# Performance work log

Measured on AMD Instinct MI355X. Metric: run time of the kernel, lower is better.

Reference implementation:

```python
import jax, jax.numpy as jnp
import numpy as np

NB, DIN, DOUT = 4, 1024, 256
B, S = 8, 2048

def setup_inputs() -> dict:
    key = jax.random.key(0)
    ks = jax.random.split(key, 9)
    sd_in = 1.0 / np.sqrt(DIN)
    sd_cat = 1.0 / np.sqrt(DOUT * NB)
    return {
        'x':  jax.random.normal(ks[0], (B, S, DIN), jnp.float32),
        'Wq': jax.random.normal(ks[1], (NB, DIN, DOUT), jnp.float32) * sd_in,
        'bq': jax.random.normal(ks[2], (NB, DOUT), jnp.float32) * 0.01,
        'Wk': jax.random.normal(ks[3], (NB, DIN, DOUT), jnp.float32) * sd_in,
        'bk': jax.random.normal(ks[4], (NB, DOUT), jnp.float32) * 0.01,
        'Wv': jax.random.normal(ks[5], (NB, DIN, DOUT), jnp.float32) * sd_in,
        'bv': jax.random.normal(ks[6], (NB, DOUT), jnp.float32) * 0.01,
        'Wo': jax.random.normal(ks[7], (NB * DOUT, DOUT), jnp.float32) * sd_cat,
        'bo': jnp.zeros((DOUT,), jnp.float32),
    }

def reference(x, Wq, bq, Wk, bk, Wv, bv, Wo, bo):
    # Per-block linear projections, all blocks vectorized: [nb, b, s, d]
    Q = jnp.einsum('bsi,nio->nbso', x, Wq) + bq[:, None, None, :]
    K = jnp.einsum('bsi,nio->nbso', x, Wk) + bk[:, None, None, :]
    V = jnp.einsum('bsi,nio->nbso', x, Wv) + bv[:, None, None, :]
    scale = 1.0 / np.sqrt(DOUT)
    scores = jnp.einsum('nbso,nbto->nbst', Q, K) * scale  # [nb,b,s,s]
    weights = jax.nn.softmax(scores, axis=-1)
    attn = jnp.einsum('nbst,nbto->nbso', weights, V)       # [nb,b,s,d]
    # concat blocks along last dim: [b,s,nb*d]
    combined = jnp.transpose(attn, (1, 2, 0, 3)).reshape(attn.shape[1], attn.shape[2], -1)
    return combined @ Wo + bo
```

## Files before the change

### kernel.cpp

```cpp
#include <hip/hip_runtime.h>
#include <hip/hip_bf16.h>

typedef __attribute__((ext_vector_type(8))) short bf16x8;
typedef __attribute__((ext_vector_type(4))) float f32x4;
typedef __attribute__((ext_vector_type(16))) float f32x16;

#define DEVI __device__ __forceinline__

DEVI unsigned short f2bf(float f) {
  union { float f; unsigned u; } v; v.f = f;
  unsigned r = v.u + 0x7FFFu + ((v.u >> 16) & 1u);
  return (unsigned short)(r >> 16);
}

DEVI unsigned cvtpk(float lo, float hi) {
  unsigned r;
  asm("v_cvt_pk_bf16_f32 %0, %1, %2" : "=v"(r) : "v"(lo), "v"(hi));
  return r;
}

DEVI void gload16(const void* g, void* l) {
  __builtin_amdgcn_global_load_lds(
      (const __attribute__((address_space(1))) unsigned int*)g,
      (__attribute__((address_space(3))) unsigned int*)l, 16, 0, 0);
}

__global__ void k_prep(const float* __restrict__ x, unsigned short* __restrict__ xb,
                       const float* __restrict__ Wq, const float* __restrict__ Wk,
                       const float* __restrict__ Wv, const float* __restrict__ Wo,
                       unsigned short* __restrict__ Wt, unsigned short* __restrict__ Wot) {
  __shared__ float t[32][33];
  int bid = blockIdx.x;
  if (bid < 2048) {
    int i = bid * 256 + threadIdx.x;
    const int stride = 2048 * 256;
#pragma unroll
    for (int it = 0; it < 8; ++it, i += stride) {
      float4 v = ((const float4*)x)[i];
      ushort4 o;
      o.x = f2bf(v.x); o.y = f2bf(v.y); o.z = f2bf(v.z); o.w = f2bf(v.w);
      ((ushort4*)xb)[i] = o;
    }
  } else {
    int b2 = bid - 2048;
    int z = b2 >> 8, rem = b2 & 255;
    int r0 = (rem >> 3) * 32, c0 = (rem & 7) * 32;
    const float* in = z < 4 ? Wq : (z < 8 ? Wk : (z < 12 ? Wv : Wo));
    size_t ibase = (size_t)(z < 12 ? (z & 3) : 0) * 262144;
    unsigned short* out = z < 12 ? (Wt + (size_t)z * 262144) : Wot;
    int tx = threadIdx.x & 31, ty = threadIdx.x >> 5;
    for (int i = 0; i < 32; i += 8)
      t[ty + i][tx] = in[ibase + (size_t)(r0 + ty + i) * 256 + (c0 + tx)];
    __syncthreads();
    for (int i = 0; i < 32; i += 8)
      out[(size_t)(c0 + ty + i) * 1024 + (r0 + tx)] = f2bf(t[tx][ty + i]);
  }
}

__global__ __launch_bounds__(256, 3) void k_gemmqkv(
    const unsigned short* __restrict__ A,
    const unsigned short* __restrict__ B,
    const float* __restrict__ bq, const float* __restrict__ bk,
    const float* __restrict__ bv,
    unsigned short* __restrict__ Qb, unsigned short* __restrict__ Kg,
    unsigned short* __restrict__ Vt, float qscale)
{
  __shared__ unsigned short As[128 * 64];
  __shared__ unsigned short Bs[128 * 64];
  int tid = threadIdx.x;
  int w = tid >> 6, l = tid & 63;
  int lg = l >> 4, lm = l & 15;
  int wr = w >> 1, wc = w & 1;
  int bid = blockIdx.x;
  int wg = (bid & 7) * 384 + (bid >> 3);
  int rowblk = wg / 24, colblk = wg % 24;
  int row0 = rowblk * 128, col0 = colblk * 128;

  const f32x4 fz = {0.f, 0.f, 0.f, 0.f};
  f32x4 acc[4][4];
  for (int i = 0; i < 4; i++) for (int j = 0; j < 4; j++) acc[i][j] = fz;

  for (int t = 0; t < 16; ++t) {
    int k0 = t << 6;
    __syncthreads();
#pragma unroll
    for (int j = 0; j < 4; ++j) {
      int ch = j * 256 + tid;
      int row = ch >> 3, cirp = (ch & 7) ^ (row & 7);
      gload16(A + (size_t)(row0 + row) * 1024 + k0 + cirp * 8,
              As + (size_t)(j * 256 + w * 64) * 8);
      gload16(B + (size_t)(col0 + row) * 1024 + k0 + cirp * 8,
              Bs + (size_t)(j * 256 + w * 64) * 8);
    }
    __syncthreads();
#pragma unroll
    for (int kt = 0; kt < 2; ++kt) {
      bf16x8 bfr[4];
#pragma unroll
      for (int ni = 0; ni < 4; ++ni) {
        int r = wc * 64 + ni * 16 + lm;
        bfr[ni] = *(const bf16x8*)((const char*)Bs + r * 128 + ((kt * 64 + lg * 16) ^ ((r & 7) << 4)));
      }
#pragma unroll
      for (int mi = 0; mi < 4; ++mi) {
        int r = wr * 64 + mi * 16 + lm;
        bf16x8 afr = *(const bf16x8*)((const char*)As + r * 128 + ((kt * 64 + lg * 16) ^ ((r & 7) << 4)));
#pragma unroll
        for (int ni = 0; ni < 4; ++ni)
          acc[mi][ni] = __builtin_amdgcn_mfma_f32_16x16x32_bf16(afr, bfr[ni], acc[mi][ni], 0, 0, 0);
      }
    }
  }

  int sel = col0 >> 10;
  const float* bb = sel == 0 ? bq : (sel == 1 ? bk : bv);
#pragma unroll
  for (int mi = 0; mi < 4; ++mi) {
#pragma unroll
    for (int ni = 0; ni < 4; ++ni) {
#pragma unroll
      for (int q = 0; q < 4; ++q) {
        int rg = row0 + wr * 64 + mi * 16 + lg * 4 + q;
        int cg = col0 + wc * 64 + ni * 16 + lm;
        int cl = cg & 1023;
        float val = acc[mi][ni][q] + bb[cl];
        int bI = rg >> 11, s = rg & 2047;
        int nn = cl >> 8, d = cl & 255;
        if (sel == 0) {
          Qb[(size_t)rg * 1024 + cl] = f2bf(val * qscale);
        } else if (sel == 1) {
          Kg[((size_t)((nn * 8 + bI) * 32 + (d >> 3))) * 16384 + (size_t)s * 8 + (d & 7)] = f2bf(val);
        } else {
          int t2 = s >> 6, u = s & 63;
          int p = ((u >> 4) & 3) * 2 + ((u >> 2) & 1);
          int jv = ((u >> 3) & 1) * 4 + (u & 3);
          Vt[(((size_t)(nn * 8 + bI) * 32 + t2) * 2048 + p * 256 + d) * 8 + jv] = f2bf(val);
        }
      }
    }
  }
}

__global__ __launch_bounds__(512, 2) void k_gemmo(
    const unsigned short* __restrict__ A,
    const unsigned short* __restrict__ B,
    const float* __restrict__ bias,
    float* __restrict__ Cout)
{
  __shared__ unsigned short As[64 * 64];
  __shared__ unsigned short Bs[256 * 64];
  int tid = threadIdx.x;
  int w = tid >> 6, l = tid & 63;
  int lg = l >> 4, lm = l & 15;
  int wr = w >> 2, wc = w & 3;
  int row0 = blockIdx.y * 64;

  const f32x4 fz = {0.f, 0.f, 0.f, 0.f};
  f32x4 acc[2][4];
  for (int i = 0; i < 2; i++) for (int j = 0; j < 4; j++) acc[i][j] = fz;

  for (int t = 0; t < 16; ++t) {
    int k0 = t << 6;
    __syncthreads();
    {
      int row = tid >> 3, cirp = (tid & 7) ^ (row & 7);
      gload16(A + (size_t)(row0 + row) * 1024 + k0 + cirp * 8,
              As + (size_t)(w * 64) * 8);
    }
#pragma unroll
    for (int j = 0; j < 4; ++j) {
      int ch = j * 512 + tid;
      int row = ch >> 3, cirp = (ch & 7) ^ (row & 7);
      gload16(B + (size_t)(row) * 1024 + k0 + cirp * 8,
              Bs + (size_t)(j * 512 + w * 64) * 8);
    }
    __syncthreads();
#pragma unroll
    for (int kt = 0; kt < 2; ++kt) {
      bf16x8 bfr[4];
#pragma unroll
      for (int ni = 0; ni < 4; ++ni) {
        int r = wc * 64 + ni * 16 + lm;
        bfr[ni] = *(const bf16x8*)((const char*)Bs + r * 128 + ((kt * 64 + lg * 16) ^ ((r & 7) << 4)));
      }
#pragma unroll
      for (int mi = 0; mi < 2; ++mi) {
        int r = wr * 32 + mi * 16 + lm;
        bf16x8 afr = *(const bf16x8*)((const char*)As + r * 128 + ((kt * 64 + lg * 16) ^ ((r & 7) << 4)));
#pragma unroll
        for (int ni = 0; ni < 4; ++ni)
          acc[mi][ni] = __builtin_amdgcn_mfma_f32_16x16x32_bf16(afr, bfr[ni], acc[mi][ni], 0, 0, 0);
      }
    }
  }

#pragma unroll
  for (int mi = 0; mi < 2; ++mi)
#pragma unroll
    for (int ni = 0; ni < 4; ++ni)
#pragma unroll
      for (int q = 0; q < 4; ++q) {
        int rg = row0 + wr * 32 + mi * 16 + lg * 4 + q;
        int cg = wc * 64 + ni * 16 + lm;
        Cout[(size_t)rg * 256 + cg] = acc[mi][ni][q] + bias[cg];
      }
}

__global__ __launch_bounds__(256, 2) void k_attn(
    const unsigned short* __restrict__ Qb,
    const unsigned short* __restrict__ Kg,
    const unsigned short* __restrict__ Vt,
    unsigned short* __restrict__ comb)
{
  __shared__ unsigned short Ks[2048 * 8];
  __shared__ unsigned short Vs[2048 * 8];
  __shared__ unsigned short Ps[2 * 4 * 64 * 8];

  int i = blockIdx.x;
  int c = i & 7, j = i >> 3;
  int nbb = c + 8 * (j >> 5);
  int qt = j & 31;
  int n = nbb >> 3, b = nbb & 7;
  int q0 = qt * 64;

  int tid = threadIdx.x;
  int w = tid >> 6, l = tid & 63;
  int m = l & 31, g = l >> 5;
  int qg = w & 1, dh = w >> 1;

  bf16x8 qf[16];
  if (w < 2) {
    const unsigned short* qbase = Qb + (size_t)(b * 2048 + q0 + qg * 32 + m) * 1024 + n * 256 + g * 8;
#pragma unroll
    for (int ks = 0; ks < 16; ++ks)
      qf[ks] = *(const bf16x8*)(qbase + ks * 16);
  }

  f32x16 ao[4];
#pragma unroll
  for (int dt = 0; dt < 4; ++dt)
#pragma unroll
    for (int r = 0; r < 16; ++r) ao[dt][r] = 0.f;
  float lp = 0.f;
  bf16x8 pa[4];

  const unsigned short* kbase = Kg + (size_t)(n * 8 + b) * 32 * 16384;
  const unsigned short* vbase = Vt + (size_t)(n * 8 + b) * 32 * 16384;

#pragma unroll
  for (int jj = 0; jj < 8; ++jj) {
    int gK = jj * 256 + tid;
    gload16(kbase + (size_t)(gK >> 6) * 16384 + (size_t)(gK & 63) * 8, Ks + (size_t)gK * 8);
    gload16(vbase + (size_t)gK * 8, Vs + (size_t)gK * 8);
  }
  __syncthreads();

  for (int t = 0; t < 32; ++t) {
    if (w < 2) {
      f32x16 s0, s1;
#pragma unroll
      for (int r = 0; r < 16; ++r) { s0[r] = 0.f; s1[r] = 0.f; }
      __builtin_amdgcn_s_setprio(1);
#pragma unroll
      for (int ks = 0; ks < 16; ++ks) {
        bf16x8 k0 = *(const bf16x8*)(Ks + ((2 * ks + g) * 64 + m) * 8);
        bf16x8 k1 = *(const bf16x8*)(Ks + ((2 * ks + g) * 64 + 32 + m) * 8);
        s0 = __builtin_amdgcn_mfma_f32_32x32x16_bf16(k0, qf[ks], s0, 0, 0, 0);
        s1 = __builtin_amdgcn_mfma_f32_32x32x16_bf16(k1, qf[ks], s1, 0, 0, 0);
      }
      __builtin_amdgcn_s_setprio(0);

      float p0[16], p1[16];
#pragma unroll
      for (int r = 0; r < 16; ++r) {
        p0[r] = exp2f(s0[r] - 16.0f);
        p1[r] = exp2f(s1[r] - 16.0f);
      }
      {
        float ts = 0.f;
#pragma unroll
        for (int r = 0; r < 16; ++r) ts += p0[r] + p1[r];
        lp += ts;
      }
      {
        union { unsigned u[4]; bf16x8 v; } w0, w1, w2, w3;
#pragma unroll
        for (int wd = 0; wd < 4; ++wd) {
          w0.u[wd] = cvtpk(p0[2 * wd], p0[2 * wd + 1]);
          w1.u[wd] = cvtpk(p0[8 + 2 * wd], p0[8 + 2 * wd + 1]);
          w2.u[wd] = cvtpk(p1[2 * wd], p1[2 * wd + 1]);
          w3.u[wd] = cvtpk(p1[8 + 2 * wd], p1[8 + 2 * wd + 1]);
        }
        pa[0] = w0.v; pa[1] = w1.v; pa[2] = w2.v; pa[3] = w3.v;
      }
#pragma unroll
      for (int jd = 0; jd < 4; ++jd)
        *(uint4*)(Ps + ((qg * 4 + jd) * 64 + l) * 8) = *(uint4*)&pa[jd];
    }

    __syncthreads();

    if (t < 31 && w >= 2) {
#pragma unroll
      for (int jj = 0; jj < 16; ++jj) {
        int gK = jj * 128 + (tid - 128);
        gload16(kbase + (size_t)(gK >> 6) * 16384 + ((size_t)(t + 1) * 64 + (gK & 63)) * 8,
                Ks + (size_t)gK * 8);
      }
    }

    bf16x8 pu[4];
    if (w >= 2) {
#pragma unroll
      for (int jd = 0; jd < 4; ++jd)
        *(uint4*)&pu[jd] = *(const uint4*)(Ps + ((qg * 4 + jd) * 64 + l) * 8);
    } else {
#pragma unroll
      for (int jd = 0; jd < 4; ++jd) pu[jd] = pa[jd];
    }

    __builtin_amdgcn_s_setprio(1);
#pragma unroll
    for (int dt = 0; dt < 4; ++dt) {
      int vrow = dh * 128 + dt * 32 + m;
#pragma unroll
      for (int ks2 = 0; ks2 < 4; ++ks2) {
        bf16x8 vf = *(const bf16x8*)(Vs + ((2 * ks2 + g) * 256 + vrow) * 8);
        ao[dt] = __builtin_amdgcn_mfma_f32_32x32x16_bf16(pu[ks2], vf, ao[dt], 0, 0, 0);
      }
    }
    __builtin_amdgcn_s_setprio(0);

    __syncthreads();

    if (t < 31 && w >= 2) {
#pragma unroll
      for (int jj = 0; jj < 16; ++jj) {
        int gK = jj * 128 + (tid - 128);
        gload16(vbase + (size_t)(t + 1) * 16384 + (size_t)gK * 8, Vs + (size_t)gK * 8);
      }
    }
  }

  float l_s = lp + __shfl_xor(lp, 32);
  if (w < 2) *(float*)((char*)Ps + (qg * 64 + l) * 4) = l_s;
  __syncthreads();
  if (w >= 2) l_s = *(const float*)((char*)Ps + (qg * 64 + l) * 4);

  float rinv[16];
#pragma unroll
  for (int r = 0; r < 16; ++r) {
    float lr = __shfl(l_s, 4 * g + (r & 3) + 8 * (r >> 2));
    rinv[r] = 1.f / lr;
  }
#pragma unroll
  for (int dt = 0; dt < 4; ++dt) {
    int col = n * 256 + dh * 128 + dt * 32 + m;
#pragma unroll
    for (int r = 0; r < 16; ++r) {
      int rowq = q0 + qg * 32 + 4 * g + (r & 3) + 8 * (r >> 2);
      comb[(size_t)(b * 2048 + rowq) * 1024 + col] = f2bf(ao[dt][r] * rinv[r]);
    }
  }
}

extern "C" void kernel_launch(void* const* d_in, const int* in_sizes, int n_in,
                              void* d_out, int out_size, void* d_ws, size_t ws_size,
                              hipStream_t stream) {
  const float* x  = (const float*)d_in[0];
  const float* Wq = (const float*)d_in[1];
  const float* bq = (const float*)d_in[2];
  const float* Wk = (const float*)d_in[3];
  const float* bk = (const float*)d_in[4];
  const float* Wv = (const float*)d_in[5];
  const float* bv = (const float*)d_in[6];
  const float* Wo = (const float*)d_in[7];
  const float* bo = (const float*)d_in[8];

  const size_t MB = 1ull << 20;
  char* ws = (char*)d_ws;
  unsigned short* xb  = (unsigned short*)(ws);
  unsigned short* Wqt = (unsigned short*)(ws + 32 * MB);
  unsigned short* Wot = (unsigned short*)(ws + 38 * MB);
  unsigned short* Qb  = (unsigned short*)(ws + 40 * MB);
  unsigned short* Kg  = (unsigned short*)(ws + 72 * MB);
  unsigned short* Vt  = (unsigned short*)(ws + 104 * MB);
  unsigned short* comb = xb;

  k_prep<<<5376, 256, 0, stream>>>(x, xb, Wq, Wk, Wv, Wo, Wqt, Wot);

  const float qscale = 0.0625f * 1.44269504088896f;
  k_gemmqkv<<<3072, 256, 0, stream>>>(xb, Wqt, bq, bk, bv, Qb, Kg, Vt, qscale);

  k_attn<<<1024, 256, 0, stream>>>(Qb, Kg, Vt, comb);

  k_gemmo<<<dim3(1, 256), 512, 0, stream>>>(comb, Wot, bo, (float*)d_out);
}
```

Measured before the change: 332.3 us.

## Warp-specialize attention into QK producer and PV consumer waves with double buffering

The attention kernel now uses 512-thread blocks with 128 query rows. Four waves compute QK^T and softmax numerators and write P into a double-buffered LDS slot. Four other waves load the K/V tiles for the next step and run P·V on the previous step's P, so the two matmul stages overlap across waves. The cost is twice the LDS (double-buffered K, V and P at about 160KB) and 8 output accumulators per consumer wave, which may limit occupancy to one block per CU. The barrier pairing between the two wave groups must line up exactly.

```diff
diff --git a/kernel.cpp b/kernel.cpp
--- a/kernel.cpp
+++ b/kernel.cpp
@@ -206,65 +206,59 @@
       }
 }
 
-__global__ __launch_bounds__(256, 2) void k_attn(
+__global__ __launch_bounds__(512) void k_attn(
     const unsigned short* __restrict__ Qb,
     const unsigned short* __restrict__ Kg,
     const unsigned short* __restrict__ Vt,
     unsigned short* __restrict__ comb)
 {
-  __shared__ unsigned short Ks[2048 * 8];
-  __shared__ unsigned short Vs[2048 * 8];
-  __shared__ unsigned short Ps[2 * 4 * 64 * 8];
+  __shared__ unsigned short Ks[2][16384];
+  __shared__ unsigned short Vs[2][16384];
+  __shared__ unsigned short Ps[2][8192];
 
   int i = blockIdx.x;
   int c = i & 7, j = i >> 3;
-  int nbb = c + 8 * (j >> 5);
-  int qt = j & 31;
+  int nbb = c + 8 * (j >> 4);
+  int qt = j & 15;
   int n = nbb >> 3, b = nbb & 7;
-  int q0 = qt * 64;
+  int q0 = qt * 128;
 
   int tid = threadIdx.x;
   int w = tid >> 6, l = tid & 63;
   int m = l & 31, g = l >> 5;
-  int qg = w & 1, dh = w >> 1;
-
-  bf16x8 qf[16];
-  if (w < 2) {
-    const unsigned short* qbase = Qb + (size_t)(b * 2048 + q0 + qg * 32 + m) * 1024 + n * 256 + g * 8;
-#pragma unroll
-    for (int ks = 0; ks < 16; ++ks)
-      qf[ks] = *(const bf16x8*)(qbase + ks * 16);
-  }
-
-  f32x16 ao[4];
-#pragma unroll
-  for (int dt = 0; dt < 4; ++dt)
-#pragma unroll
-    for (int r = 0; r < 16; ++r) ao[dt][r] = 0.f;
-  float lp = 0.f;
-  bf16x8 pa[4];
 
   const unsigned short* kbase = Kg + (size_t)(n * 8 + b) * 32 * 16384;
   const unsigned short* vbase = Vt + (size_t)(n * 8 + b) * 32 * 16384;
 
 #pragma unroll
-  for (int jj = 0; jj < 8; ++jj) {
-    int gK = jj * 256 + tid;
-    gload16(kbase + (size_t)(gK >> 6) * 16384 + (size_t)(gK & 63) * 8, Ks + (size_t)gK * 8);
-    gload16(vbase + (size_t)gK * 8, Vs + (size_t)gK * 8);
+  for (int jj = 0; jj < 4; ++jj) {
+    int gK = jj * 512 + tid;
+    gload16(kbase + (size_t)(gK >> 6) * 16384 + (size_t)(gK & 63) * 8, Ks[0] + (size_t)gK * 8);
+    gload16(vbase + (size_t)gK * 8, Vs[0] + (size_t)gK * 8);
   }
   __syncthreads();
 
-  for (int t = 0; t < 32; ++t) {
-    if (w < 2) {
+  if (w < 4) {
+    int qg = w;
+    bf16x8 qf[16];
+    {
+      const unsigned short* qbase = Qb + (size_t)(b * 2048 + q0 + qg * 32 + m) * 1024 + n * 256 + g * 8;
+#pragma unroll
+      for (int ks = 0; ks < 16; ++ks)
+        qf[ks] = *(const bf16x8*)(qbase + ks * 16);
+    }
+    float lp = 0.f;
+
+    for (int t = 0; t < 32; ++t) {
+      const unsigned short* Kc = Ks[t & 1];
       f32x16 s0, s1;
 #pragma unroll
       for (int r = 0; r < 16; ++r) { s0[r] = 0.f; s1[r] = 0.f; }
       __builtin_amdgcn_s_setprio(1);
 #pragma unroll
       for (int ks = 0; ks < 16; ++ks) {
-        bf16x8 k0 = *(const bf16x8*)(Ks + ((2 * ks + g) * 64 + m) * 8);
-        bf16x8 k1 = *(const bf16x8*)(Ks + ((2 * ks + g) * 64 + 32 + m) * 8);
+        bf16x8 k0 = *(const bf16x8*)(Kc + ((2 * ks + g) * 64 + m) * 8);
+        bf16x8 k1 = *(const bf16x8*)(Kc + ((2 * ks + g) * 64 + 32 + m) * 8);
         s0 = __builtin_amdgcn_mfma_f32_32x32x16_bf16(k0, qf[ks], s0, 0, 0, 0);
         s1 = __builtin_amdgcn_mfma_f32_32x32x16_bf16(k1, qf[ks], s1, 0, 0, 0);
       }
@@ -291,75 +285,106 @@
           w2.u[wd] = cvtpk(p1[2 * wd], p1[2 * wd + 1]);
           w3.u[wd] = cvtpk(p1[8 + 2 * wd], p1[8 + 2 * wd + 1]);
         }
-        pa[0] = w0.v; pa[1] = w1.v; pa[2] = w2.v; pa[3] = w3.v;
-      }
+        unsigned short* Pd = Ps[t & 1];
+        *(uint4*)(Pd + ((qg * 4 + 0) * 64 + l) * 8) = *(uint4*)&w0;
+        *(uint4*)(Pd + ((qg * 4 + 1) * 64 + l) * 8) = *(uint4*)&w1;
+        *(uint4*)(Pd + ((qg * 4 + 2) * 64 + l) * 8) = *(uint4*)&w2;
+        *(uint4*)(Pd + ((qg * 4 + 3) * 64 + l) * 8) = *(uint4*)&w3;
+      }
+      __syncthreads();
+      __syncthreads();
+    }
+
+    float l_s = lp + __shfl_xor(lp, 32);
+    *(float*)((char*)Ps[0] + (qg * 64 + l) * 4) = l_s;
+    __syncthreads();
+
+  } else {
+    int qg = w - 4;
+    int cid = tid - 256;
+    f32x16 ao[8];
+#pragma unroll
+    for (int dt = 0; dt < 8; ++dt)
+#pragma unroll
+      for (int r = 0; r < 16; ++r) ao[dt][r] = 0.f;
+    bf16x8 pu[4];
+
+    for (int t = 0; t < 32; ++t) {
+      if (t < 31) {
+        unsigned short* Kd = Ks[(t + 1) & 1];
+#pragma unroll
+        for (int jj = 0; jj < 8; ++jj) {
+          int gK = jj * 256 + cid;
+          gload16(kbase + (size_t)(gK >> 6) * 16384 + ((size_t)(t + 1) * 64 + (gK & 63)) * 8,
+                  Kd + (size_t)gK * 8);
+        }
+      }
+      if (t > 0) {
+        const unsigned short* Pp = Ps[(t - 1) & 1];
+        const unsigned short* Vp = Vs[(t - 1) & 1];
+#pragma unroll
+        for (int jd = 0; jd < 4; ++jd)
+          *(uint4*)&pu[jd] = *(const uint4*)(Pp + ((qg * 4 + jd) * 64 + l) * 8);
+        __builtin_amdgcn_s_setprio(1);
+#pragma unroll
+        for (int dt = 0; dt < 8; ++dt) {
+          int vrow = dt * 32 + m;
+#pragma unroll
+          for (int ks2 = 0; ks2 < 4; ++ks2) {
+            bf16x8 vf = *(const bf16x8*)(Vp + ((2 * ks2 + g) * 256 + vrow) * 8);
+            ao[dt] = __builtin_amdgcn_mfma_f32_32x32x16_bf16(pu[ks2], vf, ao[dt], 0, 0, 0);
+          }
+        }
+        __builtin_amdgcn_s_setprio(0);
+      }
+      __syncthreads();
+
+      if (t < 31) {
+        unsigned short* Vd = Vs[(t + 1) & 1];
+#pragma unroll
+        for (int jj = 0; jj < 8; ++jj) {
+          int gK = jj * 256 + cid;
+          gload16(vbase + (size_t)(t + 1) * 16384 + (size_t)gK * 8, Vd + (size_t)gK * 8);
+        }
+      }
+      __syncthreads();
+    }
+
+    {
+      const unsigned short* Pp = Ps[1];
+      const unsigned short* Vp = Vs[1];
 #pragma unroll
       for (int jd = 0; jd < 4; ++jd)
-        *(uint4*)(Ps + ((qg * 4 + jd) * 64 + l) * 8) = *(uint4*)&pa[jd];
-    }
-
-    __syncthreads();
-
-    if (t < 31 && w >= 2) {
-#pragma unroll
-      for (int jj = 0; jj < 16; ++jj) {
-        int gK = jj * 128 + (tid - 128);
-        gload16(kbase + (size_t)(gK >> 6) * 16384 + ((size_t)(t + 1) * 64 + (gK & 63)) * 8,
-                Ks + (size_t)gK * 8);
-      }
-    }
-
-    bf16x8 pu[4];
-    if (w >= 2) {
-#pragma unroll
-      for (int jd = 0; jd < 4; ++jd)
-        *(uint4*)&pu[jd] = *(const uint4*)(Ps + ((qg * 4 + jd) * 64 + l) * 8);
-    } else {
-#pragma unroll
-      for (int jd = 0; jd < 4; ++jd) pu[jd] = pa[jd];
-    }
-
-    __builtin_amdgcn_s_setprio(1);
-#pragma unroll
-    for (int dt = 0; dt < 4; ++dt) {
-      int vrow = dh * 128 + dt * 32 + m;
-#pragma unroll
-      for (int ks2 = 0; ks2 < 4; ++ks2) {
-        bf16x8 vf = *(const bf16x8*)(Vs + ((2 * ks2 + g) * 256 + vrow) * 8);
-        ao[dt] = __builtin_amdgcn_mfma_f32_32x32x16_bf16(pu[ks2], vf, ao[dt], 0, 0, 0);
-      }
-    }
-    __builtin_amdgcn_s_setprio(0);
-
-    __syncthreads();
-
-    if (t < 31 && w >= 2) {
-#pragma unroll
-      for (int jj = 0; jj < 16; ++jj) {
-        int gK = jj * 128 + (tid - 128);
-        gload16(vbase + (size_t)(t + 1) * 16384 + (size_t)gK * 8, Vs + (size_t)gK * 8);
-      }
-    }
-  }
-
-  float l_s = lp + __shfl_xor(lp, 32);
-  if (w < 2) *(float*)((char*)Ps + (qg * 64 + l) * 4) = l_s;
-  __syncthreads();
-  if (w >= 2) l_s = *(const float*)((char*)Ps + (qg * 64 + l) * 4);
-
-  float rinv[16];
-#pragma unroll
-  for (int r = 0; r < 16; ++r) {
-    float lr = __shfl(l_s, 4 * g + (r & 3) + 8 * (r >> 2));
-    rinv[r] = 1.f / lr;
-  }
-#pragma unroll
-  for (int dt = 0; dt < 4; ++dt) {
-    int col = n * 256 + dh * 128 + dt * 32 + m;
+        *(uint4*)&pu[jd] = *(const uint4*)(Pp + ((qg * 4 + jd) * 64 + l) * 8);
+      __builtin_amdgcn_s_setprio(1);
+#pragma unroll
+      for (int dt = 0; dt < 8; ++dt) {
+        int vrow = dt * 32 + m;
+#pragma unroll
+        for (int ks2 = 0; ks2 < 4; ++ks2) {
+          bf16x8 vf = *(const bf16x8*)(Vp + ((2 * ks2 + g) * 256 + vrow) * 8);
+          ao[dt] = __builtin_amdgcn_mfma_f32_32x32x16_bf16(pu[ks2], vf, ao[dt], 0, 0, 0);
+        }
+      }
+      __builtin_amdgcn_s_setprio(0);
+    }
+    __syncthreads();
+
+    float l_s = *(const float*)((const char*)Ps[0] + (qg * 64 + l) * 4);
+    float rinv[16];
 #pragma unroll
     for (int r = 0; r < 16; ++r) {
-      int rowq = q0 + qg * 32 + 4 * g + (r & 3) + 8 * (r >> 2);
-      comb[(size_t)(b * 2048 + rowq) * 1024 + col] = f2bf(ao[dt][r] * rinv[r]);
+      float lr = __shfl(l_s, 4 * g + (r & 3) + 8 * (r >> 2));
+      rinv[r] = 1.f / lr;
+    }
+#pragma unroll
+    for (int dt = 0; dt < 8; ++dt) {
+      int col = n * 256 + dt * 32 + m;
+#pragma unroll
+      for (int r = 0; r < 16; ++r) {
+        int rowq = q0 + qg * 32 + 4 * g + (r & 3) + 8 * (r >> 2);
+        comb[(size_t)(b * 2048 + rowq) * 1024 + col] = f2bf(ao[dt][r] * rinv[r]);
+      }
     }
   }
 }
@@ -392,7 +417,7 @@
   const float qscale = 0.0625f * 1.44269504088896f;
   k_gemmqkv<<<3072, 256, 0, stream>>>(xb, Wqt, bq, bk, bv, Qb, Kg, Vt, qscale);
 
-  k_attn<<<1024, 256, 0, stream>>>(Qb, Kg, Vt, comb);
+  k_attn<<<512, 512, 0, stream>>>(Qb, Kg, Vt, comb);
 
   k_gemmo<<<dim3(1, 256), 512, 0, stream>>>(comb, Wot, bo, (float*)d_out);
 }
```

Measured after the change: 303.7 us. 1.09x faster.
